# Performance work log

Measured on AMD Instinct MI355X. Metric: run time of the kernel, lower is better.

## Reference

```python
import jax, jax.numpy as jnp
import numpy as np

DIM_MODEL = 1024
DIM_LLM = 4096
HEAD_NUM = 16
DIM_KEYS = DIM_MODEL // HEAD_NUM  # 64


def setup_inputs() -> dict:
    key = jax.random.key(0)
    ks = jax.random.split(key, 11)
    B, P, V = 8, 256, 8192
    s_q = 1.0 / np.sqrt(DIM_MODEL)
    s_l = 1.0 / np.sqrt(DIM_LLM)
    s_d = 1.0 / np.sqrt(DIM_MODEL)
    return {
        "query": jax.random.normal(ks[0], (B, P, DIM_MODEL), dtype=jnp.float32),
        "key": jax.random.normal(ks[1], (V, DIM_LLM), dtype=jnp.float32),
        "value": jax.random.normal(ks[2], (V, DIM_LLM), dtype=jnp.float32),
        "Wq": jax.random.normal(ks[3], (DIM_MODEL, DIM_MODEL), dtype=jnp.float32) * s_q,
        "bq": jnp.zeros((DIM_MODEL,), dtype=jnp.float32),
        "Wk": jax.random.normal(ks[4], (DIM_LLM, DIM_MODEL), dtype=jnp.float32) * s_l,
        "bk": jnp.zeros((DIM_MODEL,), dtype=jnp.float32),
        "Wv": jax.random.normal(ks[5], (DIM_LLM, DIM_MODEL), dtype=jnp.float32) * s_l,
        "bv": jnp.zeros((DIM_MODEL,), dtype=jnp.float32),
        "Wo": jax.random.normal(ks[6], (DIM_MODEL, DIM_LLM), dtype=jnp.float32) * s_d,
        "bo": jnp.zeros((DIM_LLM,), dtype=jnp.float32),
    }


def reference(query, key, value, Wq, bq, Wk, bk, Wv, bv, Wo, bo):
    B, P, _ = query.shape
    V = key.shape[0]
    # projections
    q = (query @ Wq + bq).reshape(B, P, HEAD_NUM, DIM_KEYS)        # [b,p,h,k]
    k = (key @ Wk + bk).reshape(V, HEAD_NUM, DIM_KEYS)             # [v,h,k]
    v = (value @ Wv + bv).reshape(V, HEAD_NUM, DIM_KEYS)           # [v,h,k]
    scale = 1.0 / DIM_KEYS  # NOTE: original uses 1/d_k, not 1/sqrt(d_k)
    scores = jnp.einsum('bphk,vhk->bhpv', q, k)                    # [b,h,p,v]
    A = jax.nn.softmax(scale * scores, axis=-1)                    # dropout is identity in eval
    mapped = jnp.einsum('bhpv,vhk->bphk', A, v)                    # [b,p,h,k]
    mapped = mapped.reshape(B, P, HEAD_NUM * DIM_KEYS)
    return mapped @ Wo + bo                                        # [b,p,dim_llm]
```

## Files before the change

kernel.cpp:

```cpp
#include <hip/hip_runtime.h>


typedef __attribute__((ext_vector_type(8)))  short          short8;
typedef __attribute__((ext_vector_type(4)))  short          short4v;
typedef __attribute__((ext_vector_type(4)))  float          f32x4;
typedef __attribute__((ext_vector_type(16))) float          f32x16;
typedef __attribute__((ext_vector_type(8)))  unsigned short ushort8;

__device__ __forceinline__ unsigned short f2bf(float f) {
    unsigned int u = __builtin_bit_cast(unsigned int, f);
    u += 0x7fffu + ((u >> 16) & 1u);
    return (unsigned short)(u >> 16);
}

__device__ __forceinline__ void gld_lds16(const ushort* g, ushort* l) {
    __builtin_amdgcn_global_load_lds(
        (const __attribute__((address_space(1))) void*)g,
        (__attribute__((address_space(3))) void*)l, 16, 0, 0);
}

__global__ __launch_bounds__(256) void conv_f32_bf16(
    const float* __restrict__ in, ushort* __restrict__ out, int n)
{
    int i = (blockIdx.x * 256 + threadIdx.x) * 8;
    if (i >= n) return;
    float4 a = *(const float4*)(in + i);
    float4 b = *(const float4*)(in + i + 4);
    ushort8 o = {f2bf(a.x), f2bf(a.y), f2bf(a.z), f2bf(a.w),
                 f2bf(b.x), f2bf(b.y), f2bf(b.z), f2bf(b.w)};
    *(ushort8*)(out + i) = o;
}

__global__ __launch_bounds__(256) void transconv(
    const float* __restrict__ in, ushort* __restrict__ out, int R, int C)
{
    __shared__ float t[32][33];
    const int tx = threadIdx.x & 31, ty = threadIdx.x >> 5;
    const int bx = blockIdx.x, by = blockIdx.y;
#pragma unroll
    for (int i = 0; i < 4; ++i)
        t[ty + 8 * i][tx] = in[(size_t)(by * 32 + ty + 8 * i) * C + bx * 32 + tx];
    __syncthreads();
#pragma unroll
    for (int i = 0; i < 4; ++i)
        out[(size_t)(bx * 32 + ty + 8 * i) * R + by * 32 + tx] = f2bf(t[tx][ty + 8 * i]);
}

template<int OUT_BF16, int BIAS_ROW>
__global__ __launch_bounds__(256) void gemm_bt(
    const ushort* __restrict__ A, const ushort* __restrict__ BT,
    const float* __restrict__ bias, void* __restrict__ Cout,
    int M, int N, int K, float oscale)
{
    __shared__ ushort As[128 * 32];
    __shared__ ushort Bs[128 * 32];
    const int tid = threadIdx.x;
    const int w = tid >> 6, lane = tid & 63;
    const int m = lane & 15, quad = lane >> 4;
    const int wr = w >> 1, wc = w & 1;
    const int bx = blockIdx.x, by = blockIdx.y;

    f32x4 acc[4][4];
#pragma unroll
    for (int i = 0; i < 4; ++i)
#pragma unroll
        for (int j = 0; j < 4; ++j)
#pragma unroll
            for (int r = 0; r < 4; ++r) acc[i][j][r] = 0.f;

    const int r_i = lane >> 2;
    const int ccl = (lane & 3) ^ ((lane >> 2) & 3) ^ quad;
    const ushort* Ag = A  + (size_t)(by * 128 + w * 32 + r_i) * K + ccl * 8;
    const ushort* Bg = BT + (size_t)(bx * 128 + w * 32 + r_i) * K + ccl * 8;
    ushort* AsW = As + w * 1024;
    ushort* BsW = Bs + w * 1024;
    const size_t rowstep = (size_t)16 * K;

    const int phys = (quad ^ (m & 3) ^ (m >> 2)) * 8;
    int aoff[4], boff[4];
#pragma unroll
    for (int i = 0; i < 4; ++i) {
        aoff[i] = (wr * 64 + i * 16 + m) * 32 + phys;
        boff[i] = (wc * 64 + i * 16 + m) * 32 + phys;
    }

    const int kIters = K >> 5;
    for (int kt = 0; kt < kIters; ++kt) {
        __syncthreads();
        gld_lds16(Ag, AsW);
        gld_lds16(Ag + rowstep, AsW + 512);
        gld_lds16(Bg, BsW);
        gld_lds16(Bg + rowstep, BsW + 512);
        Ag += 32; Bg += 32;
        __syncthreads();
        short8 af[4], bf[4];
#pragma unroll
        for (int i = 0; i < 4; ++i) af[i] = *(const short8*)(As + aoff[i]);
#pragma unroll
        for (int i = 0; i < 4; ++i) bf[i] = *(const short8*)(Bs + boff[i]);
#pragma unroll
        for (int i = 0; i < 4; ++i)
#pragma unroll
            for (int j = 0; j < 4; ++j)
                acc[i][j] = __builtin_amdgcn_mfma_f32_16x16x32_bf16(
                    af[i], bf[j], acc[i][j], 0, 0, 0);
    }

    const int row0 = by * 128 + wr * 64;
    const int col0 = bx * 128 + wc * 64;
#pragma unroll
    for (int i = 0; i < 4; ++i) {
#pragma unroll
        for (int j = 0; j < 4; ++j) {
            const int c = col0 + j * 16 + m;
            float bcol = BIAS_ROW ? 0.f : bias[c];
#pragma unroll
            for (int r = 0; r < 4; ++r) {
                const int rw = row0 + i * 16 + quad * 4 + r;
                float v = acc[i][j][r] + (BIAS_ROW ? bias[rw] : bcol);
                v *= oscale;
                if (OUT_BF16)
                    ((ushort*)Cout)[(size_t)rw * N + c] = f2bf(v);
                else
                    ((float*)Cout)[(size_t)rw * N + c] = v;
            }
        }
    }
}

__global__ __launch_bounds__(128) void attn_mfma(
    const ushort* __restrict__ qb, const ushort* __restrict__ kb,
    const ushort* __restrict__ vT, ushort* __restrict__ mappedb)
{
    __shared__ ushort Qs[64 * 64];
    __shared__ ushort Ks[128 * 64];
    __shared__ ushort Vs[64 * 128];
    __shared__ short  Ps[64 * 136];

    const int tid = threadIdx.x;
    const int w = tid >> 6, lane = tid & 63;
    const int l31 = lane & 31, l5 = lane >> 5, quad = lane >> 4;
    const int idx = blockIdx.x;
    const int pt = idx & 3, h = (idx >> 2) & 15, b = idx >> 6;
    const int pbase = b * 256 + pt * 64;

    const int c8 = lane & 7, r8 = lane >> 3, c16 = lane & 15;

#pragma unroll
    for (int j = 0; j < 4; ++j) {
        const int t = w * 4 + j;
        const ushort* g = qb + (size_t)(pbase + t * 8 + r8) * 1024 + h * 64 + c8 * 8;
        gld_lds16(g, Qs + t * 512);
    }
    __syncthreads();
    short8 qf[4];
#pragma unroll
    for (int ks = 0; ks < 4; ++ks)
        qf[ks] = *(const short8*)(Qs + (w * 32 + l31) * 64 + ks * 16 + l5 * 8);

    f32x16 o[2];
#pragma unroll
    for (int dt = 0; dt < 2; ++dt)
#pragma unroll
        for (int r = 0; r < 16; ++r) o[dt][r] = 0.f;
    float lpart = 0.f;

    const int ccK = c8 ^ r8;
    const int prow = (w * 32 + l31) * 136;

    for (int vt = 0; vt < 8192; vt += 128) {
        __syncthreads();
#pragma unroll
        for (int i = 0; i < 8; ++i) {
            const int t = w * 8 + i;
            const ushort* gk = kb + (size_t)(vt + t * 8 + r8) * 1024 + h * 64 + ccK * 8;
            gld_lds16(gk, Ks + t * 512);
            const int d_l = t * 4 + quad;
            const int ccV = c16 ^ (d_l & 15);
            const ushort* gv = vT + (size_t)(h * 64 + d_l) * 8192 + vt + ccV * 8;
            gld_lds16(gv, Vs + t * 512);
        }
        __syncthreads();

        f32x16 st[4];
#pragma unroll
        for (int v4 = 0; v4 < 4; ++v4)
#pragma unroll
            for (int r = 0; r < 16; ++r) st[v4][r] = 0.f;
#pragma unroll
        for (int v4 = 0; v4 < 4; ++v4) {
            const int row = (v4 * 32 + l31) * 64;
            const int sw = l31 & 7;
#pragma unroll
            for (int ks = 0; ks < 4; ++ks) {
                const int ph = ((ks * 2 + l5) ^ sw) * 8;
                short8 kf = *(const short8*)(Ks + row + ph);
                st[v4] = __builtin_amdgcn_mfma_f32_32x32x16_bf16(kf, qf[ks], st[v4], 0, 0, 0);
            }
        }

#pragma unroll
        for (int v4 = 0; v4 < 4; ++v4) {
#pragma unroll
            for (int g = 0; g < 4; ++g) {
                float e0 = exp2f(st[v4][g * 4 + 0]);
                float e1 = exp2f(st[v4][g * 4 + 1]);
                float e2 = exp2f(st[v4][g * 4 + 2]);
                float e3 = exp2f(st[v4][g * 4 + 3]);
                lpart += (e0 + e1) + (e2 + e3);
                short4v pk = {(short)f2bf(e0), (short)f2bf(e1),
                              (short)f2bf(e2), (short)f2bf(e3)};
                *(short4v*)(Ps + prow + v4 * 32 + g * 8 + l5 * 4) = pk;
            }
        }
        __syncthreads();

#pragma unroll
        for (int k8 = 0; k8 < 8; ++k8) {
            short8 pf = *(const short8*)(Ps + prow + k8 * 16 + l5 * 8);
#pragma unroll
            for (int dt = 0; dt < 2; ++dt) {
                const int d_l = dt * 32 + l31;
                const int ph = ((k8 * 2 + l5) ^ (d_l & 15)) * 8;
                short8 vf = *(const short8*)(Vs + d_l * 128 + ph);
                o[dt] = __builtin_amdgcn_mfma_f32_32x32x16_bf16(pf, vf, o[dt], 0, 0, 0);
            }
        }
    }

    float lfull = lpart + __shfl_xor(lpart, 32, 64);
    float rinv = 1.0f / lfull;
#pragma unroll
    for (int r = 0; r < 16; ++r) {
        const int poff = (r & 3) + 8 * (r >> 2) + 4 * l5;
        const float sc = __shfl(rinv, poff, 64);
        const size_t grow = (size_t)(pbase + w * 32 + poff) * 1024;
#pragma unroll
        for (int dt = 0; dt < 2; ++dt)
            mappedb[grow + h * 64 + dt * 32 + l31] = f2bf(o[dt][r] * sc);
    }
}

extern "C" void kernel_launch(void* const* d_in, const int* in_sizes, int n_in,
                              void* d_out, int out_size, void* d_ws, size_t ws_size,
                              hipStream_t stream)
{
    const float* query = (const float*)d_in[0];
    const float* key   = (const float*)d_in[1];
    const float* value = (const float*)d_in[2];
    const float* Wq    = (const float*)d_in[3];
    const float* bq    = (const float*)d_in[4];
    const float* Wk    = (const float*)d_in[5];
    const float* bk    = (const float*)d_in[6];
    const float* Wv    = (const float*)d_in[7];
    const float* bv    = (const float*)d_in[8];
    const float* Wo    = (const float*)d_in[9];
    const float* bo    = (const float*)d_in[10];
    float* out = (float*)d_out;

    char* ws = (char*)d_ws;
    ushort* tmpb    = (ushort*)ws;
    ushort* wslot   = (ushort*)(ws + (64ull << 20));
    ushort* queryb  = (ushort*)(ws + (72ull << 20));
    ushort* qb      = (ushort*)(ws + (76ull << 20));
    ushort* mappedb = (ushort*)ws;
    ushort* kb      = (ushort*)d_out;
    ushort* vT      = (ushort*)((char*)d_out + (16ull << 20));

    const float QSCALE = 1.4426950408889634f / 64.0f;

    conv_f32_bf16<<<16384, 256, 0, stream>>>(key, tmpb, 8192 * 4096);
    transconv<<<dim3(32, 128), 256, 0, stream>>>(Wk, wslot, 4096, 1024);
    gemm_bt<1, 0><<<dim3(8, 64), 256, 0, stream>>>(tmpb, wslot, bk, kb,
                                                   8192, 1024, 4096, 1.0f);
    conv_f32_bf16<<<16384, 256, 0, stream>>>(value, tmpb, 8192 * 4096);
    transconv<<<dim3(32, 128), 256, 0, stream>>>(Wv, wslot, 4096, 1024);
    gemm_bt<1, 1><<<dim3(64, 8), 256, 0, stream>>>(wslot, tmpb, bv, vT,
                                                   1024, 8192, 4096, 1.0f);
    conv_f32_bf16<<<1024, 256, 0, stream>>>(query, queryb, 2048 * 1024);
    transconv<<<dim3(32, 32), 256, 0, stream>>>(Wq, wslot, 1024, 1024);
    gemm_bt<1, 0><<<dim3(8, 16), 256, 0, stream>>>(queryb, wslot, bq, qb,
                                                   2048, 1024, 1024, QSCALE);
    attn_mfma<<<512, 128, 0, stream>>>(qb, kb, vT, mappedb);
    transconv<<<dim3(128, 32), 256, 0, stream>>>(Wo, wslot, 1024, 4096);
    gemm_bt<0, 0><<<dim3(32, 16), 256, 0, stream>>>(mappedb, wslot, bo, out,
                                                    2048, 4096, 1024, 1.0f);
}
```

Measured before the change: 819.4 us.

## Split attention key tiles across four waves with LDS reduction of partial outputs

The attention kernel now uses 256 threads per block instead of 128. Each pair of waves shares a 32-row query slice and splits the 128-key tile between them. Each wave computes half the scores and half the PV products, and the partial outputs and row sums are combined through LDS at the end. The intra-tile syncthreads before PV is replaced by an lgkmcnt wait, which relies on each wave reading only its own Ps rows. Other changes: s_setprio around the MFMA blocks and packed bf16 conversion via v_cvt_pk_bf16_f32. The aim is more waves per CU to hide latency, at the cost of an extra reduction and more LDS traffic.

```diff
diff --git a/kernel.cpp b/kernel.cpp
--- a/kernel.cpp
+++ b/kernel.cpp
@@ -2,10 +2,10 @@
 
 
 typedef __attribute__((ext_vector_type(8)))  short          short8;
-typedef __attribute__((ext_vector_type(4)))  short          short4v;
 typedef __attribute__((ext_vector_type(4)))  float          f32x4;
 typedef __attribute__((ext_vector_type(16))) float          f32x16;
 typedef __attribute__((ext_vector_type(8)))  unsigned short ushort8;
+typedef __attribute__((ext_vector_type(2)))  unsigned int   uint2v;
 
 __device__ __forceinline__ unsigned short f2bf(float f) {
     unsigned int u = __builtin_bit_cast(unsigned int, f);
@@ -128,7 +128,7 @@
     }
 }
 
-__global__ __launch_bounds__(128) void attn_mfma(
+__global__ __launch_bounds__(256, 2) void attn_mfma(
     const ushort* __restrict__ qb, const ushort* __restrict__ kb,
     const ushort* __restrict__ vT, ushort* __restrict__ mappedb)
 {
@@ -140,6 +140,7 @@
     const int tid = threadIdx.x;
     const int w = tid >> 6, lane = tid & 63;
     const int l31 = lane & 31, l5 = lane >> 5, quad = lane >> 4;
+    const int wp = w >> 1, wv = w & 1;
     const int idx = blockIdx.x;
     const int pt = idx & 3, h = (idx >> 2) & 15, b = idx >> 6;
     const int pbase = b * 256 + pt * 64;
@@ -147,8 +148,8 @@
     const int c8 = lane & 7, r8 = lane >> 3, c16 = lane & 15;
 
 #pragma unroll
-    for (int j = 0; j < 4; ++j) {
-        const int t = w * 4 + j;
+    for (int j = 0; j < 2; ++j) {
+        const int t = w * 2 + j;
         const ushort* g = qb + (size_t)(pbase + t * 8 + r8) * 1024 + h * 64 + c8 * 8;
         gld_lds16(g, Qs + t * 512);
     }
@@ -156,7 +157,7 @@
     short8 qf[4];
 #pragma unroll
     for (int ks = 0; ks < 4; ++ks)
-        qf[ks] = *(const short8*)(Qs + (w * 32 + l31) * 64 + ks * 16 + l5 * 8);
+        qf[ks] = *(const short8*)(Qs + (wp * 32 + l31) * 64 + ks * 16 + l5 * 8);
 
     f32x16 o[2];
 #pragma unroll
@@ -166,13 +167,13 @@
     float lpart = 0.f;
 
     const int ccK = c8 ^ r8;
-    const int prow = (w * 32 + l31) * 136;
+    const int prow = (wp * 32 + l31) * 136;
 
     for (int vt = 0; vt < 8192; vt += 128) {
         __syncthreads();
 #pragma unroll
-        for (int i = 0; i < 8; ++i) {
-            const int t = w * 8 + i;
+        for (int i = 0; i < 4; ++i) {
+            const int t = w * 4 + i;
             const ushort* gk = kb + (size_t)(vt + t * 8 + r8) * 1024 + h * 64 + ccK * 8;
             gld_lds16(gk, Ks + t * 512);
             const int d_l = t * 4 + quad;
@@ -182,41 +183,50 @@
         }
         __syncthreads();
 
-        f32x16 st[4];
-#pragma unroll
-        for (int v4 = 0; v4 < 4; ++v4)
-#pragma unroll
-            for (int r = 0; r < 16; ++r) st[v4][r] = 0.f;
-#pragma unroll
-        for (int v4 = 0; v4 < 4; ++v4) {
+        f32x16 st[2];
+#pragma unroll
+        for (int s = 0; s < 2; ++s)
+#pragma unroll
+            for (int r = 0; r < 16; ++r) st[s][r] = 0.f;
+        __builtin_amdgcn_s_setprio(1);
+#pragma unroll
+        for (int s = 0; s < 2; ++s) {
+            const int v4 = wv * 2 + s;
             const int row = (v4 * 32 + l31) * 64;
             const int sw = l31 & 7;
 #pragma unroll
             for (int ks = 0; ks < 4; ++ks) {
                 const int ph = ((ks * 2 + l5) ^ sw) * 8;
                 short8 kf = *(const short8*)(Ks + row + ph);
-                st[v4] = __builtin_amdgcn_mfma_f32_32x32x16_bf16(kf, qf[ks], st[v4], 0, 0, 0);
+                st[s] = __builtin_amdgcn_mfma_f32_32x32x16_bf16(kf, qf[ks], st[s], 0, 0, 0);
             }
         }
-
-#pragma unroll
-        for (int v4 = 0; v4 < 4; ++v4) {
+        __builtin_amdgcn_s_setprio(0);
+
+#pragma unroll
+        for (int s = 0; s < 2; ++s) {
+            const int v4 = wv * 2 + s;
 #pragma unroll
             for (int g = 0; g < 4; ++g) {
-                float e0 = exp2f(st[v4][g * 4 + 0]);
-                float e1 = exp2f(st[v4][g * 4 + 1]);
-                float e2 = exp2f(st[v4][g * 4 + 2]);
-                float e3 = exp2f(st[v4][g * 4 + 3]);
+                float e0 = exp2f(st[s][g * 4 + 0]);
+                float e1 = exp2f(st[s][g * 4 + 1]);
+                float e2 = exp2f(st[s][g * 4 + 2]);
+                float e3 = exp2f(st[s][g * 4 + 3]);
                 lpart += (e0 + e1) + (e2 + e3);
-                short4v pk = {(short)f2bf(e0), (short)f2bf(e1),
-                              (short)f2bf(e2), (short)f2bf(e3)};
-                *(short4v*)(Ps + prow + v4 * 32 + g * 8 + l5 * 4) = pk;
+                unsigned int plo, phi;
+                asm("v_cvt_pk_bf16_f32 %0, %1, %2" : "=v"(plo) : "v"(e0), "v"(e1));
+                asm("v_cvt_pk_bf16_f32 %0, %1, %2" : "=v"(phi) : "v"(e2), "v"(e3));
+                uint2v pk = {plo, phi};
+                *(uint2v*)(Ps + prow + v4 * 32 + g * 8 + l5 * 4) = pk;
             }
         }
-        __syncthreads();
-
-#pragma unroll
-        for (int k8 = 0; k8 < 8; ++k8) {
+        asm volatile("s_waitcnt lgkmcnt(0)" ::: "memory");
+        __builtin_amdgcn_sched_barrier(0);
+
+        __builtin_amdgcn_s_setprio(1);
+#pragma unroll
+        for (int k4 = 0; k4 < 4; ++k4) {
+            const int k8 = wv * 4 + k4;
             short8 pf = *(const short8*)(Ps + prow + k8 * 16 + l5 * 8);
 #pragma unroll
             for (int dt = 0; dt < 2; ++dt) {
@@ -226,18 +236,40 @@
                 o[dt] = __builtin_amdgcn_mfma_f32_32x32x16_bf16(pf, vf, o[dt], 0, 0, 0);
             }
         }
-    }
-
-    float lfull = lpart + __shfl_xor(lpart, 32, 64);
-    float rinv = 1.0f / lfull;
-#pragma unroll
-    for (int r = 0; r < 16; ++r) {
-        const int poff = (r & 3) + 8 * (r >> 2) + 4 * l5;
-        const float sc = __shfl(rinv, poff, 64);
-        const size_t grow = (size_t)(pbase + w * 32 + poff) * 1024;
+        __builtin_amdgcn_s_setprio(0);
+    }
+
+    __syncthreads();
+    float* Red  = (float*)Ks;
+    float* Lred = (float*)Vs;
+    if (wv == 1) {
 #pragma unroll
         for (int dt = 0; dt < 2; ++dt)
-            mappedb[grow + h * 64 + dt * 32 + l31] = f2bf(o[dt][r] * sc);
+#pragma unroll
+            for (int r = 0; r < 16; ++r)
+                Red[wp * 2048 + (dt * 16 + r) * 64 + lane] = o[dt][r];
+        Lred[wp * 64 + lane] = lpart;
+    }
+    __syncthreads();
+    if (wv == 0) {
+#pragma unroll
+        for (int dt = 0; dt < 2; ++dt)
+#pragma unroll
+            for (int r = 0; r < 16; ++r)
+                o[dt][r] += Red[wp * 2048 + (dt * 16 + r) * 64 + lane];
+        lpart += Lred[wp * 64 + lane];
+
+        float lfull = lpart + __shfl_xor(lpart, 32, 64);
+        float rinv = 1.0f / lfull;
+#pragma unroll
+        for (int r = 0; r < 16; ++r) {
+            const int poff = (r & 3) + 8 * (r >> 2) + 4 * l5;
+            const float sc = __shfl(rinv, poff, 64);
+            const size_t grow = (size_t)(pbase + wp * 32 + poff) * 1024;
+#pragma unroll
+            for (int dt = 0; dt < 2; ++dt)
+                mappedb[grow + h * 64 + dt * 32 + l31] = f2bf(o[dt][r] * sc);
+        }
     }
 }
 
@@ -281,7 +313,7 @@
     transconv<<<dim3(32, 32), 256, 0, stream>>>(Wq, wslot, 1024, 1024);
     gemm_bt<1, 0><<<dim3(8, 16), 256, 0, stream>>>(queryb, wslot, bq, qb,
                                                    2048, 1024, 1024, QSCALE);
-    attn_mfma<<<512, 128, 0, stream>>>(qb, kb, vT, mappedb);
+    attn_mfma<<<512, 256, 0, stream>>>(qb, kb, vT, mappedb);
     transconv<<<dim3(128, 32), 256, 0, stream>>>(Wo, wslot, 1024, 4096);
     gemm_bt<0, 0><<<dim3(32, 16), 256, 0, stream>>>(mappedb, wslot, bo, out,
                                                     2048, 4096, 1024, 1.0f);
```

Result: faster. 722.7 us (-11.8%).
